# Kernel optimization log

Measured on AMD Instinct MI355X. Metric: run time of the kernel, lower is better.

Reference implementation:

```python
import jax, jax.numpy as jnp
import numpy as np

SCALE = 100.0
TOPK_IDX_THRESH = 10  # original compares argsort *indices* (not ranks) to 10, replicated faithfully


def setup_inputs() -> dict:
    key = jax.random.key(0)
    k1, k2, k3 = jax.random.split(key, 3)
    feature = jax.random.normal(k1, (4096, 1024), dtype=jnp.float32)
    query = jax.random.normal(k2, (1000, 1024), dtype=jnp.float32)
    target = jax.random.randint(k3, (4096,), 0, 1000, dtype=jnp.int64)
    return {"feature": feature, "query": query, "target": target}


def reference(feature, query, target):
    B = feature.shape[0]
    f = feature / jnp.linalg.norm(feature, axis=1, keepdims=True)  # [B, D]
    q = query / jnp.linalg.norm(query, axis=1, keepdims=True)      # [C, D]
    pred_base = f @ q.T                                            # [B, C]

    # masked_select(pred.T [C,B], label [C,B]) flattens row-major over classes,
    # so the selected per-sample logits come out ordered by (target[b], b).
    perm = jnp.argsort(target)  # stable sort -> ties broken by index, matching flatten order
    pred_sel = pred_base[perm, target[perm]][:, None]              # [B, 1]

    label_matrix = target[:, None] == target[None, :]              # [B, B]
    feature_s = (f @ f.T) * (~label_matrix)                        # [B, B]
    sorted_idx = jnp.argsort(-feature_s, axis=-1)                  # descending argsort indices
    nn_label_matrix = (sorted_idx < TOPK_IDX_THRESH).astype(f.dtype)  # [B, B]

    # Equivalent of repeat + masked_select + view: pred_nn_mat[b, i] = pred_base[i, target[b]]
    pred_nn_mat = pred_base[:, target].T                           # [B, B]
    pred_nn = jnp.mean(pred_nn_mat @ nn_label_matrix, axis=1, keepdims=True)  # [B, 1]

    logits = jnp.concatenate([pred_sel, pred_nn], axis=1)          # [B, 2]
    # nll_loss with all-zero labels == mean of -log_softmax[:, 0]
    loss = jnp.mean(-jax.nn.log_softmax(SCALE * logits, axis=1)[:, 0])
    return loss
```

## Files before the change

kernel.cpp:

```cpp
#include <hip/hip_runtime.h>
#include <math.h>

#define BB 4096
#define CC 1000
#define DD 1024
#define NRB 512
#define SCALEF 100.0f

__device__ inline float wred(float v) {
#pragma unroll
    for (int o = 32; o > 0; o >>= 1) v += __shfl_down(v, o);
    return v;
}

__device__ inline float dot4(float4 a, float4 b) {
    return a.x * b.x + a.y * b.y + a.z * b.z + a.w * b.w;
}

union K1Shared {
    float accW[4][DD];
    struct {
        unsigned short tgt[BB];
        unsigned short ord[BB];
        int wcnt[4][1024];
        int wsum[4];
    } sort;
};

__global__ __launch_bounds__(256) void k1(const float* __restrict__ feature,
                                          const float* __restrict__ query,
                                          const int* __restrict__ target,
                                          float* __restrict__ p,
                                          float* __restrict__ part,
                                          int* __restrict__ order,
                                          int* __restrict__ startsg,
                                          int* __restrict__ cntsg) {
    __shared__ K1Shared u;
    int tid = threadIdx.x, lane = tid & 63, wv = tid >> 6, bid = blockIdx.x;

    if (bid == NRB) {
        for (int i = tid; i < BB; i += 256) u.sort.tgt[i] = (unsigned short)target[i];
        for (int i = tid; i < 4096; i += 256) ((int*)u.sort.wcnt)[i] = 0;
        __syncthreads();
        {
            int base_i = wv * 1024;
            for (int r = 0; r < 16; ++r) {
                int c = u.sort.tgt[base_i + r * 64 + lane];
                atomicAdd(&u.sort.wcnt[wv][c], 1);
            }
        }
        __syncthreads();

        {
            int b4 = tid * 4;
            int w0[4], w1[4], w2[4], w3[4], t[4];
#pragma unroll
            for (int j = 0; j < 4; ++j) {
                int c = b4 + j;
                w0[j] = u.sort.wcnt[0][c];
                w1[j] = u.sort.wcnt[1][c];
                w2[j] = u.sort.wcnt[2][c];
                w3[j] = u.sort.wcnt[3][c];
                t[j] = w0[j] + w1[j] + w2[j] + w3[j];
            }
            int tot = t[0] + t[1] + t[2] + t[3];
            int inc = tot;
#pragma unroll
            for (int off = 1; off < 64; off <<= 1) {
                int s = __shfl_up(inc, off);
                if (lane >= off) inc += s;
            }
            if (lane == 63) u.sort.wsum[wv] = inc;
            __syncthreads();
            int wpre = 0;
            for (int w = 0; w < wv; ++w) wpre += u.sort.wsum[w];
            int excl = wpre + inc - tot;
            int pref = 0;
#pragma unroll
            for (int j = 0; j < 4; ++j) {
                int c = b4 + j;
                int e = excl + pref;
                pref += t[j];
                startsg[c] = e;
                cntsg[c] = t[j];
                u.sort.wcnt[0][c] = e;
                u.sort.wcnt[1][c] = e + w0[j];
                u.sort.wcnt[2][c] = e + w0[j] + w1[j];
                u.sort.wcnt[3][c] = e + w0[j] + w1[j] + w2[j];
            }
        }
        __syncthreads();

        {
            int base_i = wv * 1024;
            for (int r = 0; r < 16; ++r) {
                int idx = base_i + r * 64 + lane;
                int c = u.sort.tgt[idx];
                unsigned long long mask = ~0ull;
#pragma unroll
                for (int k = 0; k < 10; ++k) {
                    unsigned long long bal = __ballot((c >> k) & 1);
                    mask &= ((c >> k) & 1) ? bal : ~bal;
                }
                int rank = __popcll(mask & ((1ull << lane) - 1ull));
                int base = u.sort.wcnt[wv][c];
                u.sort.ord[base + rank] = (unsigned short)idx;
                if (rank == 0) u.sort.wcnt[wv][c] = base + __popcll(mask);
            }
        }
        __syncthreads();

        for (int i = tid; i < BB; i += 256) order[i] = (int)u.sort.ord[i];
        return;
    }

    float4 acc[4];
#pragma unroll
    for (int k = 0; k < 4; ++k) acc[k] = make_float4(0.f, 0.f, 0.f, 0.f);
    int b0 = bid * 8 + wv * 2;
#pragma unroll
    for (int r = 0; r < 2; ++r) {
        int b = b0 + r;
        int tb = target[b];
        const float4* fr = (const float4*)(feature + (size_t)b * DD);
        const float4* qr = (const float4*)(query + (size_t)tb * DD);
        float4 x[4], q[4];
#pragma unroll
        for (int k = 0; k < 4; ++k) { x[k] = fr[lane + 64 * k]; q[k] = qr[lane + 64 * k]; }
        float nf = 0.f, nq = 0.f, dt = 0.f;
#pragma unroll
        for (int k = 0; k < 4; ++k) {
            nf += dot4(x[k], x[k]);
            nq += dot4(q[k], q[k]);
            dt += dot4(x[k], q[k]);
        }
        nf = wred(nf); nq = wred(nq); dt = wred(dt);
        nf = __shfl(nf, 0); nq = __shfl(nq, 0); dt = __shfl(dt, 0);
        float rn = rsqrtf(nf);
        if (lane == 0) p[b] = dt * rn * rsqrtf(nq);
#pragma unroll
        for (int k = 0; k < 4; ++k) {
            acc[k].x += x[k].x * rn; acc[k].y += x[k].y * rn;
            acc[k].z += x[k].z * rn; acc[k].w += x[k].w * rn;
        }
    }
#pragma unroll
    for (int k = 0; k < 4; ++k)
        ((float4*)&u.accW[wv][0])[lane + 64 * k] = acc[k];
    __syncthreads();
    {
        float4 a0 = ((const float4*)u.accW[0])[tid];
        float4 a1 = ((const float4*)u.accW[1])[tid];
        float4 a2 = ((const float4*)u.accW[2])[tid];
        float4 a3 = ((const float4*)u.accW[3])[tid];
        float4 s;
        s.x = a0.x + a1.x + a2.x + a3.x;
        s.y = a0.y + a1.y + a2.y + a3.y;
        s.z = a0.z + a1.z + a2.z + a3.z;
        s.w = a0.w + a1.w + a2.w + a3.w;
        ((float4*)part)[bid * 256 + tid] = s;
    }
}

__global__ __launch_bounds__(256) void k2(const float* __restrict__ part,
                                          float* __restrict__ part2) {
    const float4* part4 = (const float4*)part;
    int g = blockIdx.x, tid = threadIdx.x;
    float4 a = make_float4(0.f, 0.f, 0.f, 0.f);
#pragma unroll 8
    for (int blk = g * 32; blk < g * 32 + 32; ++blk) {
        float4 v = part4[blk * 256 + tid];
        a.x += v.x; a.y += v.y; a.z += v.z; a.w += v.w;
    }
    ((float4*)part2)[g * 256 + tid] = a;
}

__global__ __launch_bounds__(256) void k3(const float* __restrict__ query,
                                          const float* __restrict__ part2,
                                          const float* __restrict__ p,
                                          const int* __restrict__ order,
                                          const int* __restrict__ startsg,
                                          const int* __restrict__ cntsg,
                                          float* __restrict__ lossp) {
    __shared__ float red[4][2];
    __shared__ float rbc[4];
    int c = blockIdx.x, tid = threadIdx.x, lane = tid & 63, wv = tid >> 6;

    const float4* p2 = (const float4*)part2;
    float4 s = make_float4(0.f, 0.f, 0.f, 0.f);
#pragma unroll
    for (int k = 0; k < 16; ++k) {
        float4 v = p2[k * 256 + tid];
        s.x += v.x; s.y += v.y; s.z += v.z; s.w += v.w;
    }
    float4 q = ((const float4*)(query + (size_t)c * DD))[tid];
    float nq = dot4(q, q);
    float dt = dot4(q, s);
    nq = wred(nq); dt = wred(dt);
    if (lane == 0) { red[wv][0] = nq; red[wv][1] = dt; }
    __syncthreads();
    nq = red[0][0] + red[1][0] + red[2][0] + red[3][0];
    dt = red[0][1] + red[1][1] + red[2][1] + red[3][1];
    float nn = (10.0f / (float)BB) * dt * rsqrtf(nq);

    int s0 = startsg[c], n = cntsg[c];
    float partl = 0.f;
    for (int j = tid; j < n; j += 256) {
        int i = order[s0 + j];
        int oi = order[i];
        float d = SCALEF * (nn - p[oi]);
        partl += (d > 0.f) ? (d + log1pf(expf(-d))) : log1pf(expf(d));
    }
    partl = wred(partl);
    if (lane == 0) rbc[wv] = partl;
    __syncthreads();
    if (tid == 0) lossp[c] = rbc[0] + rbc[1] + rbc[2] + rbc[3];
}

__global__ __launch_bounds__(256) void k4(const float* __restrict__ lossp,
                                          float* __restrict__ out) {
    __shared__ float rbc[4];
    int tid = threadIdx.x, lane = tid & 63, wv = tid >> 6;
    float a = 0.f;
    for (int j = tid; j < CC; j += 256) a += lossp[j];
    a = wred(a);
    if (lane == 0) rbc[wv] = a;
    __syncthreads();
    if (tid == 0) out[0] = (rbc[0] + rbc[1] + rbc[2] + rbc[3]) / (float)BB;
}

extern "C" void kernel_launch(void* const* d_in, const int* in_sizes, int n_in,
                              void* d_out, int out_size, void* d_ws, size_t ws_size,
                              hipStream_t stream) {
    const float* feature = (const float*)d_in[0];
    const float* query   = (const float*)d_in[1];
    const int*   target  = (const int*)d_in[2];
    float* out = (float*)d_out;
    float* ws  = (float*)d_ws;

    float* p       = ws;
    int*   order   = (int*)(ws + 4096);
    int*   startsg = (int*)(ws + 8192);
    int*   cntsg   = (int*)(ws + 9216);
    float* lossp   = ws + 10240;
    float* part    = ws + 16384;
    float* part2   = ws + 16384 + 512 * 1024;

    k1<<<NRB + 1, 256, 0, stream>>>(feature, query, target, p, part, order, startsg, cntsg);
    k2<<<16, 256, 0, stream>>>(part, part2);
    k3<<<CC, 256, 0, stream>>>(query, part2, p, order, startsg, cntsg, lossp);
    k4<<<1, 256, 0, stream>>>(lossp, out);
}
```

Measured before the change: 28.49 us.

## Fold sort block into main grid and fully reduce column sums in k2

```diff
diff --git a/kernel.cpp b/kernel.cpp
--- a/kernel.cpp
+++ b/kernel.cpp
@@ -4,7 +4,7 @@
 #define BB 4096
 #define CC 1000
 #define DD 1024
-#define NRB 512
+#define NBLK 512
 #define SCALEF 100.0f
 
 __device__ inline float wred(float v) {
@@ -38,7 +38,7 @@
     __shared__ K1Shared u;
     int tid = threadIdx.x, lane = tid & 63, wv = tid >> 6, bid = blockIdx.x;
 
-    if (bid == NRB) {
+    if (bid == NBLK - 1) {
         for (int i = tid; i < BB; i += 256) u.sort.tgt[i] = (unsigned short)target[i];
         for (int i = tid; i < 4096; i += 256) ((int*)u.sort.wcnt)[i] = 0;
         __syncthreads();
@@ -111,6 +111,7 @@
         __syncthreads();
 
         for (int i = tid; i < BB; i += 256) order[i] = (int)u.sort.ord[i];
+        ((float4*)part)[(NBLK - 1) * 256 + tid] = make_float4(0.f, 0.f, 0.f, 0.f);
         return;
     }
 
@@ -118,9 +119,13 @@
 #pragma unroll
     for (int k = 0; k < 4; ++k) acc[k] = make_float4(0.f, 0.f, 0.f, 0.f);
     int b0 = bid * 8 + wv * 2;
-#pragma unroll
-    for (int r = 0; r < 2; ++r) {
-        int b = b0 + r;
+    int rows[3];
+    rows[0] = b0; rows[1] = b0 + 1;
+    int nr = 2;
+    if (bid < 8 && wv == 0) { rows[2] = 4088 + bid; nr = 3; }
+
+    for (int r = 0; r < nr; ++r) {
+        int b = rows[r];
         int tb = target[b];
         const float4* fr = (const float4*)(feature + (size_t)b * DD);
         const float4* qr = (const float4*)(query + (size_t)tb * DD);
@@ -163,20 +168,36 @@
 }
 
 __global__ __launch_bounds__(256) void k2(const float* __restrict__ part,
-                                          float* __restrict__ part2) {
-    const float4* part4 = (const float4*)part;
+                                          float* __restrict__ S) {
+    __shared__ float4 red[256];
+    const float4* p4 = (const float4*)part;
     int g = blockIdx.x, tid = threadIdx.x;
+    int fc = g * 8 + (tid & 7);
+    int rg = tid >> 3;
     float4 a = make_float4(0.f, 0.f, 0.f, 0.f);
-#pragma unroll 8
-    for (int blk = g * 32; blk < g * 32 + 32; ++blk) {
-        float4 v = part4[blk * 256 + tid];
+#pragma unroll
+    for (int i = 0; i < 16; ++i) {
+        int r = rg + 32 * i;
+        float4 v = p4[r * 256 + fc];
         a.x += v.x; a.y += v.y; a.z += v.z; a.w += v.w;
     }
-    ((float4*)part2)[g * 256 + tid] = a;
+    red[tid] = a;
+    __syncthreads();
+#pragma unroll
+    for (int s = 16; s >= 1; s >>= 1) {
+        if (rg < s) {
+            float4 o = red[tid + s * 8];
+            float4 m = red[tid];
+            m.x += o.x; m.y += o.y; m.z += o.z; m.w += o.w;
+            red[tid] = m;
+        }
+        __syncthreads();
+    }
+    if (tid < 8) ((float4*)S)[g * 8 + tid] = red[tid];
 }
 
 __global__ __launch_bounds__(256) void k3(const float* __restrict__ query,
-                                          const float* __restrict__ part2,
+                                          const float* __restrict__ S,
                                           const float* __restrict__ p,
                                           const int* __restrict__ order,
                                           const int* __restrict__ startsg,
@@ -186,13 +207,7 @@
     __shared__ float rbc[4];
     int c = blockIdx.x, tid = threadIdx.x, lane = tid & 63, wv = tid >> 6;
 
-    const float4* p2 = (const float4*)part2;
-    float4 s = make_float4(0.f, 0.f, 0.f, 0.f);
-#pragma unroll
-    for (int k = 0; k < 16; ++k) {
-        float4 v = p2[k * 256 + tid];
-        s.x += v.x; s.y += v.y; s.z += v.z; s.w += v.w;
-    }
+    float4 s = ((const float4*)S)[tid];
     float4 q = ((const float4*)(query + (size_t)c * DD))[tid];
     float nq = dot4(q, q);
     float dt = dot4(q, s);
@@ -243,11 +258,11 @@
     int*   startsg = (int*)(ws + 8192);
     int*   cntsg   = (int*)(ws + 9216);
     float* lossp   = ws + 10240;
+    float* S       = ws + 11264;
     float* part    = ws + 16384;
-    float* part2   = ws + 16384 + 512 * 1024;
-
-    k1<<<NRB + 1, 256, 0, stream>>>(feature, query, target, p, part, order, startsg, cntsg);
-    k2<<<16, 256, 0, stream>>>(part, part2);
-    k3<<<CC, 256, 0, stream>>>(query, part2, p, order, startsg, cntsg, lossp);
+
+    k1<<<NBLK, 256, 0, stream>>>(feature, query, target, p, part, order, startsg, cntsg);
+    k2<<<32, 256, 0, stream>>>(part, S);
+    k3<<<CC, 256, 0, stream>>>(query, S, p, order, startsg, cntsg, lossp);
     k4<<<1, 256, 0, stream>>>(lossp, out);
 }
```

Result: faster. 25.96 us (-8.9%).
